# Kernel optimization log

Measured on AMD Instinct MI355X. Metric: run time of the kernel, lower is better.

The kernel has to match this reference:

```python
import jax, jax.numpy as jnp
import numpy as np
from jax import lax

C = 256
HEADS = 8
H2 = HEADS // 2          # heads per branch
HD = C // HEADS          # head dim = 32
SR = 4                   # spatial reduction ratio
WS = 7                   # window size (hard-coded in source)
SCALE = HD ** -0.5
EPS = 1e-5


def _window_partition(t, H, W, D):
    # t: [B, h, N, c] -> [B*h*nW, WS^3, c]
    B, h, N, c = t.shape
    t = t.reshape(B * h, H // WS, WS, W // WS, WS, D // WS, WS, c)
    t = t.transpose(0, 1, 3, 5, 2, 4, 6, 7)
    return t.reshape(-1, WS * WS * WS, c)


def _window_reverse(w, H, W, D, head):
    # w: [BH*nW, WS^3, c] -> [B, N, head*c] (heads interleaved into channels)
    nW = (H // WS) * (W // WS) * (D // WS)
    BH = w.shape[0] // nW
    x = w.reshape(BH, H // WS, W // WS, D // WS, WS, WS, WS, -1)
    x = x.transpose(0, 1, 4, 2, 5, 3, 6, 7).reshape(BH, H, W, D, -1)
    B = BH // head
    x = x.reshape(B, head, H, W, D, -1).transpose(0, 2, 3, 4, 1, 5)
    return x.reshape(B, H * W * D, -1)


def setup_inputs() -> dict:
    key = jax.random.key(0)
    ks = jax.random.split(key, 16)
    B, H, W, D = 1, 28, 28, 28
    N = H * W * D
    tn = lambda k, shp: jax.random.normal(k, shp, jnp.float32) * 0.02
    # conv fan-out inits (per source _init_weights)
    lepe_fan = 3 * 3 * C // C  # depthwise: groups=C
    sr_fan = SR * SR * C
    return {
        "x": jax.random.normal(ks[0], (B, N, C), jnp.float32),
        "H": H, "W": W, "D": D,
        "lepe_w": tn(ks[1], (C, C)),
        "lepe_b": jnp.zeros((C,), jnp.float32),
        "lepe_conv_w": jax.random.normal(ks[2], (C, 1, 3, 3, 3), jnp.float32) * np.sqrt(2.0 / lepe_fan),
        "lepe_conv_b": jnp.zeros((C,), jnp.float32),
        "sr_w": jax.random.normal(ks[3], (C, C, SR, SR, SR), jnp.float32) * np.sqrt(2.0 / sr_fan),
        "sr_b": jnp.zeros((C,), jnp.float32),
        "norm_g": jnp.ones((C,), jnp.float32),
        "norm_b": jnp.zeros((C,), jnp.float32),
        "q1_w": tn(ks[4], (C // 2, C)),
        "kv1_w": tn(ks[5], (C, C)),
        "q2_w": tn(ks[6], (C // 2, C)),
        "kv2_w": tn(ks[7], (C, C)),
        "proj_w": tn(ks[8], (C, C)),
        "proj_b": jnp.zeros((C,), jnp.float32),
    }


def _forward(x, lepe_w, lepe_b, lepe_conv_w, lepe_conv_b, sr_w, sr_b,
             norm_g, norm_b, q1_w, kv1_w, q2_w, kv2_w, proj_w, proj_b,
             H, W, D):
    B, N, _ = x.shape
    # --- LePE: linear -> depthwise Conv3d over (H,W,D) ---
    y = x @ lepe_w.T + lepe_b                              # [B,N,C]
    y = y.transpose(0, 2, 1).reshape(B, C, H, W, D)
    lepe = lax.conv_general_dilated(
        y, lepe_conv_w, window_strides=(1, 1, 1), padding='SAME',
        dimension_numbers=('NCDHW', 'OIDHW', 'NCDHW'), feature_group_count=C)
    lepe = (lepe + lepe_conv_b[None, :, None, None, None])
    lepe = lepe.reshape(B, C, N).transpose(0, 2, 1)        # [B,N,C]

    x_ = x.transpose(0, 2, 1).reshape(B, C, H, W, D)

    # --- Branch 1: spatially-reduced global attention (heads 0..3) ---
    q1 = (x @ q1_w.T).reshape(B, N, H2, HD).transpose(0, 2, 1, 3)   # [B,h2,N,hd]
    x1 = lax.conv_general_dilated(
        x_, sr_w, window_strides=(SR, SR, SR), padding='VALID',
        dimension_numbers=('NCDHW', 'OIDHW', 'NCDHW'))
    x1 = x1 + sr_b[None, :, None, None, None]
    x1 = x1.reshape(B, C, -1).transpose(0, 2, 1)                    # [B,Nr,C]
    mu = x1.mean(-1, keepdims=True)
    var = ((x1 - mu) ** 2).mean(-1, keepdims=True)
    x1 = (x1 - mu) * lax.rsqrt(var + EPS) * norm_g + norm_b
    x1 = jax.nn.gelu(x1, approximate=False)
    Nr = x1.shape[1]
    kv1 = (x1 @ kv1_w.T).reshape(B, Nr, 2, H2, HD).transpose(2, 0, 3, 1, 4)
    k1, v1 = kv1[0], kv1[1]                                         # [B,h2,Nr,hd]
    attn1 = jax.nn.softmax(jnp.einsum('bhnd,bhmd->bhnm', q1, k1) * SCALE, axis=-1)
    o1 = jnp.einsum('bhnm,bhmd->bhnd', attn1, v1)
    o1 = o1.transpose(0, 2, 1, 3).reshape(B, N, C // 2)

    # --- Branch 2: windowed local attention (heads 4..7) ---
    q2 = (x @ q2_w.T).reshape(B, N, H2, HD).transpose(0, 2, 1, 3)
    kv2 = (x @ kv2_w.T).reshape(B, N, 2, H2, HD).transpose(2, 0, 3, 1, 4)
    k2, v2 = kv2[0], kv2[1]                                         # [B,h2,N,hd]
    q2w = _window_partition(q2, H, W, D)
    k2w = _window_partition(k2, H, W, D)
    v2w = _window_partition(v2, H, W, D)
    attn2 = jax.nn.softmax(jnp.einsum('wnd,wmd->wnm', q2w, k2w) * SCALE, axis=-1)
    o2 = jnp.einsum('wnm,wmd->wnd', attn2, v2w)
    o2 = _window_reverse(o2, H, W, D, H2)                           # [B,N,C/2]

    out = jnp.concatenate([o1, o2], axis=-1)
    return (out + lepe) @ proj_w.T + proj_b


def reference(x, H, W, D, lepe_w, lepe_b, lepe_conv_w, lepe_conv_b,
              sr_w, sr_b, norm_g, norm_b, q1_w, kv1_w, q2_w, kv2_w,
              proj_w, proj_b):
    return _forward(x, lepe_w, lepe_b, lepe_conv_w, lepe_conv_b, sr_w, sr_b,
                    norm_g, norm_b, q1_w, kv1_w, q2_w, kv2_w, proj_w, proj_b,
                    int(H), int(W), int(D))
```

## Files before the change

kernel.cpp:

```cpp
#include <hip/hip_runtime.h>

#define N_TOK 21952
#define NR    343
#define ATT_SCALE 0.17677669529663687f

typedef unsigned short u16;
typedef short  v8s __attribute__((ext_vector_type(8)));
typedef float  v4f __attribute__((ext_vector_type(4)));

__device__ __forceinline__ float bf2f(unsigned u) {
    return __builtin_bit_cast(float, u << 16);
}
__device__ __forceinline__ u16 f2bf(float f) {
    unsigned u = __builtin_bit_cast(unsigned, f);
    u += 0x7fffu + ((u >> 16) & 1u);
    return (u16)(u >> 16);
}
__device__ __forceinline__ unsigned bfadd2(unsigned a, unsigned b) {
    float lo = bf2f(a & 0xffffu) + bf2f(b & 0xffffu);
    float hi = bf2f(a >> 16)     + bf2f(b >> 16);
    return (unsigned)f2bf(lo) | ((unsigned)f2bf(hi) << 16);
}

__global__ __launch_bounds__(256) void convert_x_kernel(
    const float* __restrict__ x, u16* __restrict__ xb)
{
    size_t i = ((size_t)blockIdx.x * 256 + threadIdx.x) * 8;
    float4 a0 = *(const float4*)(x + i);
    float4 a1 = *(const float4*)(x + i + 4);
    uint4 av;
    av.x = (unsigned)f2bf(a0.x) | ((unsigned)f2bf(a0.y) << 16);
    av.y = (unsigned)f2bf(a0.z) | ((unsigned)f2bf(a0.w) << 16);
    av.z = (unsigned)f2bf(a1.x) | ((unsigned)f2bf(a1.y) << 16);
    av.w = (unsigned)f2bf(a1.z) | ((unsigned)f2bf(a1.w) << 16);
    *(uint4*)(xb + i) = av;
}

#define WSEG0 16384
#define WSEG1 24576
#define WSEG2 32768
#define WSEG3 49152
#define WSEG4 65536
#define WSEG5 81920
#define WSEG6 82112

__global__ __launch_bounds__(256) void convert_w_kernel(
    const float* __restrict__ wl,  const float* __restrict__ wq1,
    const float* __restrict__ wq2, const float* __restrict__ wk2,
    const float* __restrict__ wk1, const float* __restrict__ wp,
    const float* __restrict__ lepe_b,
    u16* wb_comb, u16* wb_k1, u16* wb_p, float* bias_all)
{
    int gid = blockIdx.x * 256 + threadIdx.x;
    if (gid >= WSEG6) return;
    if (gid >= WSEG5) {
        int b = gid - WSEG5;
        float4 v;
        int i = b * 4;
        v.x = (i + 0 < 256) ? lepe_b[i + 0] : 0.f;
        v.y = (i + 1 < 256) ? lepe_b[i + 1] : 0.f;
        v.z = (i + 2 < 256) ? lepe_b[i + 2] : 0.f;
        v.w = (i + 3 < 256) ? lepe_b[i + 3] : 0.f;
        *(float4*)(bias_all + i) = v;
        return;
    }
    const float* s; u16* d; int l; float sc = 1.f;
    if      (gid < WSEG0) { s = wl;  d = wb_comb;           l = gid; }
    else if (gid < WSEG1) { s = wq1; d = wb_comb + 65536;   l = gid - WSEG0; sc = ATT_SCALE; }
    else if (gid < WSEG2) { s = wq2; d = wb_comb + 98304;   l = gid - WSEG1; sc = ATT_SCALE; }
    else if (gid < WSEG3) { s = wk2; d = wb_comb + 131072;  l = gid - WSEG2; }
    else if (gid < WSEG4) { s = wk1; d = wb_k1;             l = gid - WSEG3; }
    else                  { s = wp;  d = wb_p;              l = gid - WSEG4; }
    float4 v = *(const float4*)(s + (size_t)l * 4);
    *(ushort4*)(d + (size_t)l * 4) =
        make_ushort4(f2bf(v.x * sc), f2bf(v.y * sc), f2bf(v.z * sc), f2bf(v.w * sc));
}

__global__ __launch_bounds__(256) void convert_sr_kernel(
    const float* __restrict__ wsr, u16* __restrict__ wt)
{
    int u  = blockIdx.x * 256 + threadIdx.x;
    int co = u >> 8, ci = u & 255;
    const float* src = wsr + (size_t)co * 16384 + ci * 64;
#pragma unroll
    for (int t4 = 0; t4 < 16; t4++) {
        float4 v = *(const float4*)(src + t4 * 4);
        int t = t4 * 4;
        wt[(size_t)(t + 0) * 65536 + co * 256 + ci] = f2bf(v.x);
        wt[(size_t)(t + 1) * 65536 + co * 256 + ci] = f2bf(v.y);
        wt[(size_t)(t + 2) * 65536 + co * 256 + ci] = f2bf(v.z);
        wt[(size_t)(t + 3) * 65536 + co * 256 + ci] = f2bf(v.w);
    }
}

#define LDA 40

template<int BM, int BN>
__global__ __launch_bounds__(256) void gemm_bf16_t(
    const void* __restrict__ A, const u16* __restrict__ A2,
    const u16* __restrict__ W, const float* __restrict__ bias,
    void* __restrict__ outp, int M, int K, int ldout, int a_fp32, int mode)
{
    __shared__ u16 Asm[BM * LDA];
    __shared__ u16 Bsm[BN * LDA];
    const int tid = threadIdx.x;
    const int m0 = blockIdx.x * BM;
    const int n0 = blockIdx.y * BN;
    const int wave = tid >> 6, lane = tid & 63;
    constexpr int WM = BM / 2, WN = BN / 2;
    constexpr int MI = WM / 16, NJ = WN / 16;
    const int wm = (wave & 1) * WM, wn = (wave >> 1) * WN;
    const int fr = lane & 15, fq = lane >> 4;

    v4f acc[MI][NJ];
#pragma unroll
    for (int i = 0; i < MI; i++)
#pragma unroll
        for (int j = 0; j < NJ; j++) acc[i][j] = (v4f){0.f, 0.f, 0.f, 0.f};

    for (int kk = 0; kk < K; kk += 32) {
#pragma unroll
        for (int i = 0; i < BM / 64; i++) {
            int u = tid + i * 256;
            int r = u >> 2, kc = (u & 3) * 8;
            uint4 av = make_uint4(0, 0, 0, 0);
            int m = m0 + r;
            if (m < M) {
                if (a_fp32) {
                    const float* Af = (const float*)A + (size_t)m * K + kk + kc;
                    float4 a0 = *(const float4*)Af;
                    float4 a1 = *(const float4*)(Af + 4);
                    av.x = (unsigned)f2bf(a0.x) | ((unsigned)f2bf(a0.y) << 16);
                    av.y = (unsigned)f2bf(a0.z) | ((unsigned)f2bf(a0.w) << 16);
                    av.z = (unsigned)f2bf(a1.x) | ((unsigned)f2bf(a1.y) << 16);
                    av.w = (unsigned)f2bf(a1.z) | ((unsigned)f2bf(a1.w) << 16);
                } else {
                    av = *(const uint4*)((const u16*)A + (size_t)m * K + kk + kc);
                    if (A2) {
                        uint4 bv = *(const uint4*)(A2 + (size_t)m * K + kk + kc);
                        av.x = bfadd2(av.x, bv.x); av.y = bfadd2(av.y, bv.y);
                        av.z = bfadd2(av.z, bv.z); av.w = bfadd2(av.w, bv.w);
                    }
                }
            }
            *(uint4*)(Asm + r * LDA + kc) = av;
        }
#pragma unroll
        for (int i = 0; i < BN / 64; i++) {
            int u = tid + i * 256;
            int r = u >> 2, kc = (u & 3) * 8;
            uint4 wv = *(const uint4*)(W + (size_t)(n0 + r) * K + kk + kc);
            *(uint4*)(Bsm + r * LDA + kc) = wv;
        }
        __syncthreads();

        v8s af[MI], bfr[NJ];
#pragma unroll
        for (int i = 0; i < MI; i++)
            af[i] = *(const v8s*)(Asm + (wm + i * 16 + fr) * LDA + fq * 8);
#pragma unroll
        for (int j = 0; j < NJ; j++)
            bfr[j] = *(const v8s*)(Bsm + (wn + j * 16 + fr) * LDA + fq * 8);
#pragma unroll
        for (int i = 0; i < MI; i++)
#pragma unroll
            for (int j = 0; j < NJ; j++)
                acc[i][j] = __builtin_amdgcn_mfma_f32_16x16x32_bf16(
                    af[i], bfr[j], acc[i][j], 0, 0, 0);
        __syncthreads();
    }

    float* outf = (float*)outp;
    u16*   outb = (u16*)outp;
#pragma unroll
    for (int i = 0; i < MI; i++) {
#pragma unroll
        for (int j = 0; j < NJ; j++) {
            int col = n0 + wn + j * 16 + fr;
#pragma unroll
            for (int r = 0; r < 4; r++) {
                int row = m0 + wm + i * 16 + fq * 4 + r;
                if (row >= M) continue;
                float v = acc[i][j][r];
                if (bias) v += bias[col];
                if (mode == 0) outb[(size_t)row * ldout + col] = f2bf(v);
                else           outf[(size_t)row * ldout + col] = v;
            }
        }
    }
}

__global__ __launch_bounds__(256) void sr_gemm(
    const u16* __restrict__ xb, const u16* __restrict__ Wt,
    float* __restrict__ partials)
{
    __shared__ u16 Asm[128 * LDA];
    __shared__ u16 Bsm[64 * LDA];
    const int tid = threadIdx.x;
    const int m0 = blockIdx.x * 128;
    const int n0 = blockIdx.y * 64;
    const int z  = blockIdx.z;
    const int wave = tid >> 6, lane = tid & 63;
    const int wm = (wave & 1) * 64, wn = (wave >> 1) * 32;
    const int fr = lane & 15, fq = lane >> 4;

    v4f acc[4][2];
#pragma unroll
    for (int i = 0; i < 4; i++)
#pragma unroll
        for (int j = 0; j < 2; j++) acc[i][j] = (v4f){0.f, 0.f, 0.f, 0.f};

    for (int it = 0; it < 16; it++) {
        int tap = z * 2 + (it >> 3);
        int ci0 = (it & 7) * 32;
        int kz = tap >> 4, ky = (tap >> 2) & 3, kx = tap & 3;
#pragma unroll
        for (int i = 0; i < 2; i++) {
            int u = tid + i * 256;
            int r = u >> 2, seg = (u & 3) * 8;
            uint4 av = make_uint4(0, 0, 0, 0);
            int p = m0 + r;
            if (p < NR) {
                int pz = p / 49, pr = p % 49, py = pr / 7, px = pr % 7;
                int n = (pz * 4 + kz) * 784 + (py * 4 + ky) * 28 + (px * 4 + kx);
                av = *(const uint4*)(xb + (size_t)n * 256 + ci0 + seg);
            }
            *(uint4*)(Asm + r * LDA + seg) = av;
        }
        {
            int r = tid >> 2, seg = (tid & 3) * 8;
            uint4 wv = *(const uint4*)(Wt + (size_t)tap * 65536 +
                                       (size_t)(n0 + r) * 256 + ci0 + seg);
            *(uint4*)(Bsm + r * LDA + seg) = wv;
        }
        __syncthreads();

        v8s af[4], bfr[2];
#pragma unroll
        for (int i = 0; i < 4; i++)
            af[i] = *(const v8s*)(Asm + (wm + i * 16 + fr) * LDA + fq * 8);
#pragma unroll
        for (int j = 0; j < 2; j++)
            bfr[j] = *(const v8s*)(Bsm + (wn + j * 16 + fr) * LDA + fq * 8);
#pragma unroll
        for (int i = 0; i < 4; i++)
#pragma unroll
            for (int j = 0; j < 2; j++)
                acc[i][j] = __builtin_amdgcn_mfma_f32_16x16x32_bf16(
                    af[i], bfr[j], acc[i][j], 0, 0, 0);
        __syncthreads();
    }

    float* dst = partials + (size_t)z * (NR * 256);
#pragma unroll
    for (int i = 0; i < 4; i++) {
#pragma unroll
        for (int j = 0; j < 2; j++) {
            int col = n0 + wn + j * 16 + fr;
#pragma unroll
            for (int r = 0; r < 4; r++) {
                int row = m0 + wm + i * 16 + fq * 4 + r;
                if (row < NR) dst[(size_t)row * 256 + col] = acc[i][j][r];
            }
        }
    }
}

__global__ __launch_bounds__(256) void ln_gelu_kernel(
    const float* __restrict__ partials, const float* __restrict__ srb,
    const float* __restrict__ g, const float* __restrict__ b,
    u16* __restrict__ out)
{
    int row = blockIdx.x, c = threadIdx.x;
    float v = srb[c];
#pragma unroll
    for (int s = 0; s < 32; s++)
        v += partials[(size_t)s * (NR * 256) + row * 256 + c];
    float s1 = v, s2 = v * v;
#pragma unroll
    for (int off = 1; off < 64; off <<= 1) {
        s1 += __shfl_xor(s1, off);
        s2 += __shfl_xor(s2, off);
    }
    __shared__ float ws[4], ws2[4];
    int wave = c >> 6, lane = c & 63;
    if (lane == 0) { ws[wave] = s1; ws2[wave] = s2; }
    __syncthreads();
    float mean = (ws[0] + ws[1] + ws[2] + ws[3]) * (1.f / 256.f);
    float m2   = (ws2[0] + ws2[1] + ws2[2] + ws2[3]) * (1.f / 256.f);
    float var  = m2 - mean * mean;
    float xn = (v - mean) * rsqrtf(var + 1e-5f) * g[c] + b[c];
    out[row * 256 + c] = f2bf(0.5f * xn * (1.f + erff(xn * 0.70710678118654752f)));
}

__global__ __launch_bounds__(256) void dwconv_kernel(
    const u16* __restrict__ xall, const float* __restrict__ w,
    const float* __restrict__ bias, u16* __restrict__ out)
{
    __shared__ float sm[216 * 64];
    __shared__ float sw[64 * 27];
    const int tid = threadIdx.x;
    const int t  = blockIdx.x;
    const int g  = blockIdx.y;
    const int tz = t / 49, tr = t % 49, ty = tr / 7, tx = tr % 7;

    for (int u = tid; u < 64 * 27; u += 256) sw[u] = w[g * 64 * 27 + u];

    for (int u = tid; u < 216 * 8; u += 256) {
        int r = u >> 3, c8 = (u & 7) * 8;
        int vz = tz * 4 - 1 + r / 36;
        int rem = r % 36;
        int vy = ty * 4 - 1 + rem / 6;
        int vx = tx * 4 - 1 + rem % 6;
        float f[8];
        if ((unsigned)vz < 28u && (unsigned)vy < 28u && (unsigned)vx < 28u) {
            int n = vz * 784 + vy * 28 + vx;
            uint4 raw = *(const uint4*)(xall + (size_t)n * 768 + g * 64 + c8);
            f[0] = bf2f(raw.x & 0xffffu); f[1] = bf2f(raw.x >> 16);
            f[2] = bf2f(raw.y & 0xffffu); f[3] = bf2f(raw.y >> 16);
            f[4] = bf2f(raw.z & 0xffffu); f[5] = bf2f(raw.z >> 16);
            f[6] = bf2f(raw.w & 0xffffu); f[7] = bf2f(raw.w >> 16);
        } else {
#pragma unroll
            for (int i = 0; i < 8; i++) f[i] = 0.f;
        }
        float* dst = &sm[r * 64 + c8];
        *(float4*)dst       = make_float4(f[0], f[1], f[2], f[3]);
        *(float4*)(dst + 4) = make_float4(f[4], f[5], f[6], f[7]);
    }
    __syncthreads();

    const int c  = tid & 63;
    const int ch = g * 64 + c;
    float wreg[27];
#pragma unroll
    for (int j = 0; j < 27; j++) wreg[j] = sw[c * 27 + j];
    const float bc = bias[ch];

    const int vbase = (tid >> 6) * 16;
    for (int v = vbase; v < vbase + 16; v++) {
        int vz = v >> 4, vy = (v >> 2) & 3, vx = v & 3;
        float a = bc;
#pragma unroll
        for (int dz = 0; dz < 3; dz++)
#pragma unroll
            for (int dy = 0; dy < 3; dy++)
#pragma unroll
                for (int dx = 0; dx < 3; dx++)
                    a = fmaf(sm[((vz + dz) * 36 + (vy + dy) * 6 + (vx + dx)) * 64 + c],
                             wreg[dz * 9 + dy * 3 + dx], a);
        int n = (tz * 4 + vz) * 784 + (ty * 4 + vy) * 28 + (tx * 4 + vx);
        out[(size_t)n * 256 + ch] = f2bf(a);
    }
}

#define KP  40
#define VTP 360
#define PP  40

__global__ __launch_bounds__(256) void attn1_kernel(
    const u16* __restrict__ xall, const u16* __restrict__ kv1,
    u16* __restrict__ o)
{
    __shared__ u16 Ks[352 * KP];
    __shared__ u16 VTs[32 * VTP];
    __shared__ u16 Ps[4 * 16 * PP];
    const int tid = threadIdx.x;
    const int h = blockIdx.y;
    const int qbase = blockIdx.x * 352;
    const int mt0 = blockIdx.z * 11;
    const int wave = tid >> 6, lane = tid & 63;
    const int fr = lane & 15, fq = lane >> 4;

    for (int u = tid; u < 352 * 4; u += 256) {
        int r = u >> 2, seg = u & 3;
        uint4 kq = make_uint4(0, 0, 0, 0), vq = make_uint4(0, 0, 0, 0);
        if (r < NR) {
            kq = *(const uint4*)(kv1 + (size_t)r * 256 + h * 32 + seg * 8);
            vq = *(const uint4*)(kv1 + (size_t)r * 256 + 128 + h * 32 + seg * 8);
        }
        *(uint4*)(Ks + r * KP + seg * 8) = kq;
        int d0 = seg * 8;
        VTs[(d0 + 0) * VTP + r] = (u16)(vq.x & 0xffffu);
        VTs[(d0 + 1) * VTP + r] = (u16)(vq.x >> 16);
        VTs[(d0 + 2) * VTP + r] = (u16)(vq.y & 0xffffu);
        VTs[(d0 + 3) * VTP + r] = (u16)(vq.y >> 16);
        VTs[(d0 + 4) * VTP + r] = (u16)(vq.z & 0xffffu);
        VTs[(d0 + 5) * VTP + r] = (u16)(vq.z >> 16);
        VTs[(d0 + 6) * VTP + r] = (u16)(vq.w & 0xffffu);
        VTs[(d0 + 7) * VTP + r] = (u16)(vq.w >> 16);
    }
    __syncthreads();

    u16* Pw = Ps + wave * 16 * PP;
    for (int mt = mt0 + wave; mt < mt0 + 11; mt += 4) {
        int qrow = qbase + mt * 16 + fr;
        v8s aq = {0, 0, 0, 0, 0, 0, 0, 0};
        if (qrow < N_TOK)
            aq = *(const v8s*)(xall + (size_t)qrow * 768 + 256 + h * 32 + fq * 8);

        v4f s[22];
#pragma unroll
        for (int t = 0; t < 22; t++) {
            v8s bk = *(const v8s*)(Ks + (t * 16 + fr) * KP + fq * 8);
            s[t] = __builtin_amdgcn_mfma_f32_16x16x32_bf16(
                aq, bk, (v4f){0.f, 0.f, 0.f, 0.f}, 0, 0, 0);
        }
        if (fr >= 7) {
#pragma unroll
            for (int r = 0; r < 4; r++) s[21][r] = -1e30f;
        }

        float inv_l[4];
#pragma unroll
        for (int r = 0; r < 4; r++) {
            float m = s[0][r];
#pragma unroll
            for (int t = 1; t < 22; t++) m = fmaxf(m, s[t][r]);
#pragma unroll
            for (int off = 1; off < 16; off <<= 1) m = fmaxf(m, __shfl_xor(m, off));
            float l = 0.f;
#pragma unroll
            for (int t = 0; t < 22; t++) {
                v4f sv = s[t];
                float p = __expf(sv[r] - m);
                sv[r] = p; s[t] = sv;
                l += p;
            }
#pragma unroll
            for (int off = 1; off < 16; off <<= 1) l += __shfl_xor(l, off);
            inv_l[r] = 1.f / l;
        }

        v4f o0 = {0.f, 0.f, 0.f, 0.f}, o1 = {0.f, 0.f, 0.f, 0.f};
#pragma unroll
        for (int kt = 0; kt < 11; kt++) {
#pragma unroll
            for (int tt = 0; tt < 2; tt++) {
                int t = kt * 2 + tt;
#pragma unroll
                for (int r = 0; r < 4; r++)
                    Pw[(fq * 4 + r) * PP + tt * 16 + fr] = f2bf(s[t][r]);
            }
            __asm__ volatile("s_waitcnt lgkmcnt(0)" ::: "memory");
            v8s ap  = *(const v8s*)(Pw + fr * PP + fq * 8);
            v8s bv0 = *(const v8s*)(VTs + fr * VTP + kt * 32 + fq * 8);
            v8s bv1 = *(const v8s*)(VTs + (16 + fr) * VTP + kt * 32 + fq * 8);
            o0 = __builtin_amdgcn_mfma_f32_16x16x32_bf16(ap, bv0, o0, 0, 0, 0);
            o1 = __builtin_amdgcn_mfma_f32_16x16x32_bf16(ap, bv1, o1, 0, 0, 0);
        }

#pragma unroll
        for (int r = 0; r < 4; r++) {
            int n = qbase + mt * 16 + fq * 4 + r;
            if (n < N_TOK) {
                u16* op = o + (size_t)n * 256 + h * 32;
                op[fr]      = f2bf(o0[r] * inv_l[r]);
                op[16 + fr] = f2bf(o1[r] * inv_l[r]);
            }
        }
    }
}

__global__ __launch_bounds__(256) void attn2_kernel(
    const u16* __restrict__ xall, u16* __restrict__ o)
{
    __shared__ u16 Ks[352 * KP];
    __shared__ u16 VTs[32 * VTP];
    __shared__ u16 Ps[4 * 16 * PP];
    const int tid = threadIdx.x;
    const int h  = blockIdx.y;
    const int wi = blockIdx.x;
    const int zb = (wi >> 4) & 3, yb = (wi >> 2) & 3, xb = wi & 3;
    const int mt0 = blockIdx.z * 11;
    const int wave = tid >> 6, lane = tid & 63;
    const int fr = lane & 15, fq = lane >> 4;

    for (int u = tid; u < 352 * 4; u += 256) {
        int r = u >> 2, seg = u & 3;
        uint4 kq = make_uint4(0, 0, 0, 0), vq = make_uint4(0, 0, 0, 0);
        if (r < NR) {
            int mz = r / 49, mr = r % 49, my = mr / 7, mx = mr % 7;
            int nk = (zb * 7 + mz) * 784 + (yb * 7 + my) * 28 + (xb * 7 + mx);
            const u16* base = xall + (size_t)nk * 768 + 512;
            kq = *(const uint4*)(base + h * 32 + seg * 8);
            vq = *(const uint4*)(base + 128 + h * 32 + seg * 8);
        }
        *(uint4*)(Ks + r * KP + seg * 8) = kq;
        int d0 = seg * 8;
        VTs[(d0 + 0) * VTP + r] = (u16)(vq.x & 0xffffu);
        VTs[(d0 + 1) * VTP + r] = (u16)(vq.x >> 16);
        VTs[(d0 + 2) * VTP + r] = (u16)(vq.y & 0xffffu);
        VTs[(d0 + 3) * VTP + r] = (u16)(vq.y >> 16);
        VTs[(d0 + 4) * VTP + r] = (u16)(vq.z & 0xffffu);
        VTs[(d0 + 5) * VTP + r] = (u16)(vq.z >> 16);
        VTs[(d0 + 6) * VTP + r] = (u16)(vq.w & 0xffffu);
        VTs[(d0 + 7) * VTP + r] = (u16)(vq.w >> 16);
    }
    __syncthreads();

    u16* Pw = Ps + wave * 16 * PP;
    for (int mt = mt0 + wave; mt < mt0 + 11; mt += 4) {
        int tw = mt * 16 + fr;
        v8s aq = {0, 0, 0, 0, 0, 0, 0, 0};
        if (tw < NR) {
            int wz = tw / 49, tr2 = tw % 49, wy = tr2 / 7, wx = tr2 % 7;
            int nq = (zb * 7 + wz) * 784 + (yb * 7 + wy) * 28 + (xb * 7 + wx);
            aq = *(const v8s*)(xall + (size_t)nq * 768 + 384 + h * 32 + fq * 8);
        }

        v4f s[22];
#pragma unroll
        for (int t = 0; t < 22; t++) {
            v8s bk = *(const v8s*)(Ks + (t * 16 + fr) * KP + fq * 8);
            s[t] = __builtin_amdgcn_mfma_f32_16x16x32_bf16(
                aq, bk, (v4f){0.f, 0.f, 0.f, 0.f}, 0, 0, 0);
        }
        if (fr >= 7) {
#pragma unroll
            for (int r = 0; r < 4; r++) s[21][r] = -1e30f;
        }

        float inv_l[4];
#pragma unroll
        for (int r = 0; r < 4; r++) {
            float m = s[0][r];
#pragma unroll
            for (int t = 1; t < 22; t++) m = fmaxf(m, s[t][r]);
#pragma unroll
            for (int off = 1; off < 16; off <<= 1) m = fmaxf(m, __shfl_xor(m, off));
            float l = 0.f;
#pragma unroll
            for (int t = 0; t < 22; t++) {
                v4f sv = s[t];
                float p = __expf(sv[r] - m);
                sv[r] = p; s[t] = sv;
                l += p;
            }
#pragma unroll
            for (int off = 1; off < 16; off <<= 1) l += __shfl_xor(l, off);
            inv_l[r] = 1.f / l;
        }

        v4f o0 = {0.f, 0.f, 0.f, 0.f}, o1 = {0.f, 0.f, 0.f, 0.f};
#pragma unroll
        for (int kt = 0; kt < 11; kt++) {
#pragma unroll
            for (int tt = 0; tt < 2; tt++) {
                int t = kt * 2 + tt;
#pragma unroll
                for (int r = 0; r < 4; r++)
                    Pw[(fq * 4 + r) * PP + tt * 16 + fr] = f2bf(s[t][r]);
            }
            __asm__ volatile("s_waitcnt lgkmcnt(0)" ::: "memory");
            v8s ap  = *(const v8s*)(Pw + fr * PP + fq * 8);
            v8s bv0 = *(const v8s*)(VTs + fr * VTP + kt * 32 + fq * 8);
            v8s bv1 = *(const v8s*)(VTs + (16 + fr) * VTP + kt * 32 + fq * 8);
            o0 = __builtin_amdgcn_mfma_f32_16x16x32_bf16(ap, bv0, o0, 0, 0, 0);
            o1 = __builtin_amdgcn_mfma_f32_16x16x32_bf16(ap, bv1, o1, 0, 0, 0);
        }

#pragma unroll
        for (int r = 0; r < 4; r++) {
            int ts = mt * 16 + fq * 4 + r;
            if (ts < NR) {
                int wz = ts / 49, tr2 = ts % 49, wy = tr2 / 7, wx = tr2 % 7;
                int nq = (zb * 7 + wz) * 784 + (yb * 7 + wy) * 28 + (xb * 7 + wx);
                u16* op = o + (size_t)nq * 256 + 128 + h * 32;
                op[fr]      = f2bf(o0[r] * inv_l[r]);
                op[16 + fr] = f2bf(o1[r] * inv_l[r]);
            }
        }
    }
}

extern "C" void kernel_launch(void* const* d_in, const int* in_sizes, int n_in,
                              void* d_out, int out_size, void* d_ws, size_t ws_size,
                              hipStream_t stream)
{
    const float* x       = (const float*)d_in[0];
    const float* lepe_w  = (const float*)d_in[4];
    const float* lepe_b  = (const float*)d_in[5];
    const float* lconv_w = (const float*)d_in[6];
    const float* lconv_b = (const float*)d_in[7];
    const float* sr_w    = (const float*)d_in[8];
    const float* sr_b    = (const float*)d_in[9];
    const float* norm_g  = (const float*)d_in[10];
    const float* norm_b  = (const float*)d_in[11];
    const float* q1_w    = (const float*)d_in[12];
    const float* kv1_w   = (const float*)d_in[13];
    const float* q2_w    = (const float*)d_in[14];
    const float* kv2_w   = (const float*)d_in[15];
    const float* proj_w  = (const float*)d_in[16];
    const float* proj_b  = (const float*)d_in[17];
    float* out = (float*)d_out;

    const size_t NC = (size_t)N_TOK * 256;

    float* partials = (float*)d_ws;
    float* bias_all = partials + 32 * (NR * 256);
    u16* xb     = (u16*)(bias_all + 768);
    u16* xall   = xb + NC;
    u16* lepeb  = xall + (size_t)N_TOK * 768;
    u16* colb   = lepeb + NC;
    u16* x1b    = colb + NC;
    u16* kv1b   = x1b + NR * 256;
    u16* wb_comb = kv1b + NR * 256;
    u16* wb_k1  = wb_comb + 196608;
    u16* wb_p   = wb_k1 + 65536;
    u16* wsr_t  = wb_p + 65536;
    size_t need = (size_t)(32 * NR * 256 + 768) * 4 +
                  (NC + (size_t)N_TOK * 768 + 3 * NC + 2 * (size_t)NR * 256 +
                   196608 + 2 * 65536 + 4194304) * 2;
    if (ws_size < need) return;

    convert_w_kernel<<<dim3(321), 256, 0, stream>>>(
        lepe_w, q1_w, q2_w, kv2_w, kv1_w, proj_w, lepe_b,
        wb_comb, wb_k1, wb_p, bias_all);
    convert_sr_kernel<<<dim3(256), 256, 0, stream>>>(sr_w, wsr_t);
    convert_x_kernel<<<dim3(2744), 256, 0, stream>>>(x, xb);
    gemm_bf16_t<128, 64><<<dim3(172, 12), 256, 0, stream>>>(
        xb, nullptr, wb_comb, bias_all, xall, N_TOK, 256, 768, 0, 0);
    dwconv_kernel<<<dim3(343, 4), 256, 0, stream>>>(xall, lconv_w, lconv_b, lepeb);
    sr_gemm<<<dim3(3, 4, 32), 256, 0, stream>>>(xb, wsr_t, partials);
    ln_gelu_kernel<<<dim3(NR), 256, 0, stream>>>(partials, sr_b, norm_g, norm_b, x1b);
    gemm_bf16_t<64, 64><<<dim3(6, 4), 256, 0, stream>>>(
        x1b, nullptr, wb_k1, nullptr, kv1b, NR, 256, 256, 0, 0);
    attn1_kernel<<<dim3(63, 4, 2), 256, 0, stream>>>(xall, kv1b, colb);
    attn2_kernel<<<dim3(64, 4, 2), 256, 0, stream>>>(xall, colb);
    gemm_bf16_t<64, 64><<<dim3(343, 4), 256, 0, stream>>>(
        colb, lepeb, wb_p, proj_b, out, N_TOK, 256, 256, 0, 1);
}
```

Measured before the change: 276.1 us.

## Replace generic GEMM with K=256 specialised kernel using 128-wide K stages and XCD remap

```diff
diff --git a/kernel.cpp b/kernel.cpp
--- a/kernel.cpp
+++ b/kernel.cpp
@@ -93,95 +93,92 @@
     }
 }
 
-#define LDA 40
-
-template<int BM, int BN>
-__global__ __launch_bounds__(256) void gemm_bf16_t(
-    const void* __restrict__ A, const u16* __restrict__ A2,
+#define LDK 136
+
+__global__ __launch_bounds__(256, 3) void gemm_k256(
+    const u16* __restrict__ A, const u16* __restrict__ A2,
     const u16* __restrict__ W, const float* __restrict__ bias,
-    void* __restrict__ outp, int M, int K, int ldout, int a_fp32, int mode)
-{
-    __shared__ u16 Asm[BM * LDA];
-    __shared__ u16 Bsm[BN * LDA];
+    void* __restrict__ outp, int M, int ldout, int mode, int nwg, int NT)
+{
+    __shared__ u16 Asm[128 * LDK];
+    __shared__ u16 Bsm[64 * LDK];
     const int tid = threadIdx.x;
-    const int m0 = blockIdx.x * BM;
-    const int n0 = blockIdx.y * BN;
+
+    int bid = blockIdx.x;
+    int q = nwg >> 3, r = nwg & 7;
+    int xcd = bid & 7, idx = bid >> 3;
+    int wgid = (xcd < r ? xcd * (q + 1) : r * (q + 1) + (xcd - r) * q) + idx;
+    const int m0 = (wgid / NT) * 128;
+    const int n0 = (wgid % NT) * 64;
+
     const int wave = tid >> 6, lane = tid & 63;
-    constexpr int WM = BM / 2, WN = BN / 2;
-    constexpr int MI = WM / 16, NJ = WN / 16;
-    const int wm = (wave & 1) * WM, wn = (wave >> 1) * WN;
+    const int wm = (wave & 1) * 64, wn = (wave >> 1) * 32;
     const int fr = lane & 15, fq = lane >> 4;
 
-    v4f acc[MI][NJ];
-#pragma unroll
-    for (int i = 0; i < MI; i++)
-#pragma unroll
-        for (int j = 0; j < NJ; j++) acc[i][j] = (v4f){0.f, 0.f, 0.f, 0.f};
-
-    for (int kk = 0; kk < K; kk += 32) {
-#pragma unroll
-        for (int i = 0; i < BM / 64; i++) {
+    v4f acc[4][2];
+#pragma unroll
+    for (int i = 0; i < 4; i++)
+#pragma unroll
+        for (int j = 0; j < 2; j++) acc[i][j] = (v4f){0.f, 0.f, 0.f, 0.f};
+
+    for (int ph = 0; ph < 2; ph++) {
+        const int kb = ph * 128;
+#pragma unroll
+        for (int i = 0; i < 8; i++) {
             int u = tid + i * 256;
-            int r = u >> 2, kc = (u & 3) * 8;
+            int rr = u >> 4, seg = (u & 15) * 8;
             uint4 av = make_uint4(0, 0, 0, 0);
-            int m = m0 + r;
+            int m = m0 + rr;
             if (m < M) {
-                if (a_fp32) {
-                    const float* Af = (const float*)A + (size_t)m * K + kk + kc;
-                    float4 a0 = *(const float4*)Af;
-                    float4 a1 = *(const float4*)(Af + 4);
-                    av.x = (unsigned)f2bf(a0.x) | ((unsigned)f2bf(a0.y) << 16);
-                    av.y = (unsigned)f2bf(a0.z) | ((unsigned)f2bf(a0.w) << 16);
-                    av.z = (unsigned)f2bf(a1.x) | ((unsigned)f2bf(a1.y) << 16);
-                    av.w = (unsigned)f2bf(a1.z) | ((unsigned)f2bf(a1.w) << 16);
-                } else {
-                    av = *(const uint4*)((const u16*)A + (size_t)m * K + kk + kc);
-                    if (A2) {
-                        uint4 bv = *(const uint4*)(A2 + (size_t)m * K + kk + kc);
-                        av.x = bfadd2(av.x, bv.x); av.y = bfadd2(av.y, bv.y);
-                        av.z = bfadd2(av.z, bv.z); av.w = bfadd2(av.w, bv.w);
-                    }
+                av = *(const uint4*)(A + (size_t)m * 256 + kb + seg);
+                if (A2) {
+                    uint4 bv = *(const uint4*)(A2 + (size_t)m * 256 + kb + seg);
+                    av.x = bfadd2(av.x, bv.x); av.y = bfadd2(av.y, bv.y);
+                    av.z = bfadd2(av.z, bv.z); av.w = bfadd2(av.w, bv.w);
                 }
             }
-            *(uint4*)(Asm + r * LDA + kc) = av;
-        }
-#pragma unroll
-        for (int i = 0; i < BN / 64; i++) {
+            *(uint4*)(Asm + rr * LDK + seg) = av;
+        }
+#pragma unroll
+        for (int i = 0; i < 4; i++) {
             int u = tid + i * 256;
-            int r = u >> 2, kc = (u & 3) * 8;
-            uint4 wv = *(const uint4*)(W + (size_t)(n0 + r) * K + kk + kc);
-            *(uint4*)(Bsm + r * LDA + kc) = wv;
+            int rr = u >> 4, seg = (u & 15) * 8;
+            uint4 wv = *(const uint4*)(W + (size_t)(n0 + rr) * 256 + kb + seg);
+            *(uint4*)(Bsm + rr * LDK + seg) = wv;
         }
         __syncthreads();
 
-        v8s af[MI], bfr[NJ];
-#pragma unroll
-        for (int i = 0; i < MI; i++)
-            af[i] = *(const v8s*)(Asm + (wm + i * 16 + fr) * LDA + fq * 8);
-#pragma unroll
-        for (int j = 0; j < NJ; j++)
-            bfr[j] = *(const v8s*)(Bsm + (wn + j * 16 + fr) * LDA + fq * 8);
-#pragma unroll
-        for (int i = 0; i < MI; i++)
-#pragma unroll
-            for (int j = 0; j < NJ; j++)
-                acc[i][j] = __builtin_amdgcn_mfma_f32_16x16x32_bf16(
-                    af[i], bfr[j], acc[i][j], 0, 0, 0);
+#pragma unroll
+        for (int kk = 0; kk < 128; kk += 32) {
+            v8s af[4], bf[2];
+#pragma unroll
+            for (int i = 0; i < 4; i++)
+                af[i] = *(const v8s*)(Asm + (wm + i * 16 + fr) * LDK + kk + fq * 8);
+#pragma unroll
+            for (int j = 0; j < 2; j++)
+                bf[j] = *(const v8s*)(Bsm + (wn + j * 16 + fr) * LDK + kk + fq * 8);
+#pragma unroll
+            for (int i = 0; i < 4; i++)
+#pragma unroll
+                for (int j = 0; j < 2; j++)
+                    acc[i][j] = __builtin_amdgcn_mfma_f32_16x16x32_bf16(
+                        af[i], bf[j], acc[i][j], 0, 0, 0);
+        }
         __syncthreads();
     }
 
     float* outf = (float*)outp;
     u16*   outb = (u16*)outp;
 #pragma unroll
-    for (int i = 0; i < MI; i++) {
-#pragma unroll
-        for (int j = 0; j < NJ; j++) {
+    for (int i = 0; i < 4; i++) {
+#pragma unroll
+        for (int j = 0; j < 2; j++) {
             int col = n0 + wn + j * 16 + fr;
 #pragma unroll
-            for (int r = 0; r < 4; r++) {
-                int row = m0 + wm + i * 16 + fq * 4 + r;
+            for (int rr = 0; rr < 4; rr++) {
+                int row = m0 + wm + i * 16 + fq * 4 + rr;
                 if (row >= M) continue;
-                float v = acc[i][j][r];
+                float v = acc[i][j][rr];
                 if (bias) v += bias[col];
                 if (mode == 0) outb[(size_t)row * ldout + col] = f2bf(v);
                 else           outf[(size_t)row * ldout + col] = v;
@@ -189,6 +186,8 @@
         }
     }
 }
+
+#define LDA 40
 
 __global__ __launch_bounds__(256) void sr_gemm(
     const u16* __restrict__ xb, const u16* __restrict__ Wt,
@@ -619,15 +618,15 @@
         wb_comb, wb_k1, wb_p, bias_all);
     convert_sr_kernel<<<dim3(256), 256, 0, stream>>>(sr_w, wsr_t);
     convert_x_kernel<<<dim3(2744), 256, 0, stream>>>(x, xb);
-    gemm_bf16_t<128, 64><<<dim3(172, 12), 256, 0, stream>>>(
-        xb, nullptr, wb_comb, bias_all, xall, N_TOK, 256, 768, 0, 0);
+    gemm_k256<<<dim3(172 * 12), 256, 0, stream>>>(
+        xb, nullptr, wb_comb, bias_all, xall, N_TOK, 768, 0, 172 * 12, 12);
     dwconv_kernel<<<dim3(343, 4), 256, 0, stream>>>(xall, lconv_w, lconv_b, lepeb);
     sr_gemm<<<dim3(3, 4, 32), 256, 0, stream>>>(xb, wsr_t, partials);
     ln_gelu_kernel<<<dim3(NR), 256, 0, stream>>>(partials, sr_b, norm_g, norm_b, x1b);
-    gemm_bf16_t<64, 64><<<dim3(6, 4), 256, 0, stream>>>(
-        x1b, nullptr, wb_k1, nullptr, kv1b, NR, 256, 256, 0, 0);
+    gemm_k256<<<dim3(3 * 4), 256, 0, stream>>>(
+        x1b, nullptr, wb_k1, nullptr, kv1b, NR, 256, 0, 3 * 4, 4);
     attn1_kernel<<<dim3(63, 4, 2), 256, 0, stream>>>(xall, kv1b, colb);
     attn2_kernel<<<dim3(64, 4, 2), 256, 0, stream>>>(xall, colb);
-    gemm_bf16_t<64, 64><<<dim3(343, 4), 256, 0, stream>>>(
-        colb, lepeb, wb_p, proj_b, out, N_TOK, 256, 256, 0, 1);
-}
+    gemm_k256<<<dim3(172 * 4), 256, 0, stream>>>(
+        colb, lepeb, wb_p, proj_b, out, N_TOK, 256, 1, 172 * 4, 4);
+}
```

After: 284.7 us. 1.03x slower.
